# Kernel tuning notes

Measured on AMD Instinct MI355X. Metric: run time of the kernel, lower is better.

## Reference

```python
import jax, jax.numpy as jnp
import numpy as np

BEV_H, BEV_W = 200, 200
X_RANGE = (-50.0, 50.0)
Y_RANGE = (-50.0, 50.0)
IMG_W, IMG_H = 1600.0, 928.0
EPS = 1e-6


def _bev_points():
    x_half = (X_RANGE[1] - X_RANGE[0]) / (2 * BEV_W)
    y_half = (Y_RANGE[1] - Y_RANGE[0]) / (2 * BEV_H)
    xs = jnp.linspace(X_RANGE[0] + x_half, X_RANGE[1] - x_half, BEV_W)
    ys = jnp.linspace(Y_RANGE[0] + y_half, Y_RANGE[1] - y_half, BEV_H)
    gy, gx = jnp.meshgrid(ys, xs, indexing='ij')
    return jnp.stack([gx, gy, jnp.zeros_like(gx)], -1).reshape(-1, 3)  # (P,3)


def _bilinear_zeros(fm, x, y):
    # fm: (C,H,W); x,y: (P,) pixel coords; grid_sample bilinear, zeros padding, align_corners=True
    H, W = fm.shape[1], fm.shape[2]
    x0 = jnp.floor(x); y0 = jnp.floor(y)
    wx = x - x0; wy = y - y0
    def g(xi, yi):
        ok = ((xi >= 0) & (xi <= W - 1) & (yi >= 0) & (yi <= H - 1)).astype(fm.dtype)
        xc = jnp.clip(xi, 0, W - 1).astype(jnp.int32)
        yc = jnp.clip(yi, 0, H - 1).astype(jnp.int32)
        return fm[:, yc, xc] * ok  # (C,P)
    v00 = g(x0, y0); v01 = g(x0 + 1, y0); v10 = g(x0, y0 + 1); v11 = g(x0 + 1, y0 + 1)
    return v00 * (1 - wx) * (1 - wy) + v01 * wx * (1 - wy) + v10 * (1 - wx) * wy + v11 * wx * wy


def _bev_forward(feats, intrinsics, extrinsics, conv_w, conv_b, bn_gamma, bn_beta, bn_mean, bn_var):
    B, N, C, fH, fW = feats.shape
    pts = _bev_points()                                   # (P,3), z=0 ground plane
    E = jnp.linalg.inv(extrinsics)                        # T_ego->cam (B,N,4,4)
    R = E[..., :3, :3]; t = E[..., :3, 3]
    pts_cam = jnp.einsum('bnij,pj->bnpi', R, pts) + t[:, :, None, :]  # (B,N,P,3)
    depth = pts_cam[..., 2]
    p_img = jnp.einsum('bnij,bnpj->bnpi', intrinsics, pts_cam)
    u = p_img[..., 0] / (p_img[..., 2] + EPS)
    v = p_img[..., 1] / (p_img[..., 2] + EPS)
    u_feat = u * (fW / IMG_W); v_feat = v * (fH / IMG_H)
    u_norm = u_feat / (fW - 1.0) * 2.0 - 1.0
    v_norm = v_feat / (fH - 1.0) * 2.0 - 1.0
    valid = ((depth > 0.1) & (u_norm >= -1.0) & (u_norm <= 1.0)
             & (v_norm >= -1.0) & (v_norm <= 1.0)).astype(feats.dtype)  # (B,N,P)
    # align_corners=True: pixel coords recover u_feat/v_feat
    xs = (u_norm + 1.0) * 0.5 * (fW - 1.0)
    ys = (v_norm + 1.0) * 0.5 * (fH - 1.0)
    P = BEV_H * BEV_W
    bev_sum = jnp.zeros((B, C, P), feats.dtype)
    valid_sum = jnp.zeros((B, 1, P), feats.dtype)
    sample_b = jax.vmap(_bilinear_zeros)
    for cam in range(N):  # small fixed camera loop, as in original
        s = sample_b(feats[:, cam], xs[:, cam], ys[:, cam])  # (B,C,P)
        vb = valid[:, cam][:, None, :]
        bev_sum = bev_sum + s * vb
        valid_sum = valid_sum + vb
    bev = (bev_sum / (valid_sum + EPS)).reshape(B, C, BEV_H, BEV_W)
    # 1x1 conv + inference BatchNorm + ReLU
    y = jnp.einsum('oc,bchw->bohw', conv_w, bev) + conv_b[:, None, None]
    y = (y - bn_mean[:, None, None]) / jnp.sqrt(bn_var[:, None, None] + 1e-5)
    y = y * bn_gamma[:, None, None] + bn_beta[:, None, None]
    return jax.nn.relu(y)


def setup_inputs() -> dict:
    key = jax.random.key(0)
    ks = jax.random.split(key, 6)
    B, N, C, fH, fW = 4, 6, 256, 29, 50
    feats = jax.random.normal(ks[0], (B, N, C, fH, fW), jnp.float32)
    # intrinsics: realistic pinhole K
    fx = 1266.0 + 20.0 * jax.random.normal(ks[1], (B, N), jnp.float32)
    fy = 1266.0 + 20.0 * jax.random.normal(ks[2], (B, N), jnp.float32)
    z = jnp.zeros((B, N), jnp.float32); o = jnp.ones((B, N), jnp.float32)
    K = jnp.stack([jnp.stack([fx, z, 800.0 * o], -1),
                   jnp.stack([z, fy, 464.0 * o], -1),
                   jnp.stack([z, z, o], -1)], -2)  # (B,N,3,3)
    # extrinsics: proper SE(3) T_cam->ego (random rotation via QR + translation)
    A = jax.random.normal(ks[3], (B, N, 3, 3), jnp.float32)
    Q, _ = jnp.linalg.qr(A)
    Q = jnp.where(jnp.linalg.det(Q)[..., None, None] < 0, -Q, Q)
    tr = jax.random.uniform(ks[4], (B, N, 3), jnp.float32, -2.0, 2.0)
    E = jnp.zeros((B, N, 4, 4), jnp.float32)
    E = E.at[..., :3, :3].set(Q).at[..., :3, 3].set(tr).at[..., 3, 3].set(1.0)
    conv_w = 0.05 * jax.random.normal(ks[5], (C, C), jnp.float32)
    return {
        'feats': feats, 'intrinsics': K, 'extrinsics': E,
        'conv_w': conv_w, 'conv_b': jnp.zeros((C,), jnp.float32),
        'bn_gamma': jnp.ones((C,), jnp.float32), 'bn_beta': jnp.zeros((C,), jnp.float32),
        'bn_mean': jnp.zeros((C,), jnp.float32), 'bn_var': jnp.ones((C,), jnp.float32),
    }


def reference(feats, intrinsics, extrinsics, conv_w, conv_b, bn_gamma, bn_beta, bn_mean, bn_var):
    return _bev_forward(feats, intrinsics, extrinsics, conv_w, conv_b,
                        bn_gamma, bn_beta, bn_mean, bn_var)
```

## Files before the change

### kernel.cpp

```cpp
#include <hip/hip_runtime.h>
#include <hip/hip_bf16.h>


#define P_TOT  40000
#define FH     29
#define FW     50
#define NCAM   6

typedef short bf16x8 __attribute__((ext_vector_type(8)));
typedef float f32x4  __attribute__((ext_vector_type(4)));
typedef unsigned short u16x8 __attribute__((ext_vector_type(8)));

__device__ __forceinline__ float bf2f(unsigned short u) {
    union { unsigned int i; float f; } x; x.i = ((unsigned int)u) << 16; return x.f;
}
__device__ __forceinline__ unsigned short f2bf(float f) {
    union { float f; unsigned int i; } x; x.f = f;
    unsigned int i = x.i;
    return (unsigned short)((i + 0x7FFFu + ((i >> 16) & 1u)) >> 16);
}

__global__ void prep_kernel(const float* __restrict__ K, const float* __restrict__ E,
                            const float* __restrict__ convw, const float* __restrict__ convb,
                            const float* __restrict__ gamma, const float* __restrict__ beta,
                            const float* __restrict__ mean, const float* __restrict__ var,
                            float* __restrict__ params, float* __restrict__ sb,
                            unsigned short* __restrict__ wbf) {
    int idx = blockIdx.x * 256 + threadIdx.x;
    wbf[idx] = f2bf(convw[idx]);
    if (blockIdx.x != 0) return;
    int o = threadIdx.x;
    float rstd = rsqrtf(var[o] + 1e-5f);
    float s = gamma[o] * rstd;
    sb[o]       = s;
    sb[256 + o] = (convb[o] - mean[o]) * s + beta[o];
    if (o >= 24) return;
    const float* e = E + o * 16;
    const float* k = K + o * 9;
    float a00=e[0], a01=e[1], a02=e[2],  t0=e[3];
    float a10=e[4], a11=e[5], a12=e[6],  t1=e[7];
    float a20=e[8], a21=e[9], a22=e[10], t2=e[11];
    float c00 =  (a11*a22 - a12*a21);
    float c01 = -(a10*a22 - a12*a20);
    float c02 =  (a10*a21 - a11*a20);
    float det = a00*c00 + a01*c01 + a02*c02;
    float id = 1.0f / det;
    float i00 =  c00*id;
    float i01 = -(a01*a22 - a02*a21)*id;
    float i02 =  (a01*a12 - a02*a11)*id;
    float i10 =  c01*id;
    float i11 =  (a00*a22 - a02*a20)*id;
    float i12 = -(a00*a12 - a02*a10)*id;
    float i20 =  c02*id;
    float i21 = -(a00*a21 - a01*a20)*id;
    float i22 =  (a00*a11 - a01*a10)*id;
    float tp0 = -(i00*t0 + i01*t1 + i02*t2);
    float tp1 = -(i10*t0 + i11*t1 + i12*t2);
    float tp2 = -(i20*t0 + i21*t1 + i22*t2);
    float* q = params + o * 12;
    q[0] = k[0]*i00 + k[1]*i10 + k[2]*i20;
    q[1] = k[0]*i01 + k[1]*i11 + k[2]*i21;
    q[2] = k[0]*tp0 + k[1]*tp1 + k[2]*tp2;
    q[3] = k[3]*i00 + k[4]*i10 + k[5]*i20;
    q[4] = k[3]*i01 + k[4]*i11 + k[5]*i21;
    q[5] = k[3]*tp0 + k[4]*tp1 + k[5]*tp2;
    q[6] = k[6]*i00 + k[7]*i10 + k[8]*i20;
    q[7] = k[6]*i01 + k[7]*i11 + k[8]*i21;
    q[8] = k[6]*tp0 + k[7]*tp1 + k[8]*tp2;
    q[9]  = i20;
    q[10] = i21;
    q[11] = tp2;
}

__global__ __launch_bounds__(256) void transpose_kernel(const float* __restrict__ feats,
                                                        unsigned short* __restrict__ ft) {
    __shared__ unsigned short tile[256][58];
    int by = blockIdx.x;
    int t  = threadIdx.x;
    int bn = by / FH, y = by - bn * FH;
    const float* src = feats + (size_t)bn * 256 * FH * FW + y * FW;
    #pragma unroll
    for (int i = 0; i < 50; ++i) {
        int flat = i * 256 + t;
        int c = flat / 50;
        int x = flat - c * 50;
        tile[c][x] = f2bf(src[c * FH * FW + x]);
    }
    __syncthreads();
    unsigned short* dst = ft + (size_t)by * 50 * 256;
    #pragma unroll
    for (int i = 0; i < 25; ++i) {
        int flat = i * 512 + t * 2;
        int x = flat >> 8;
        int c = flat & 255;
        unsigned int v = (unsigned int)tile[c][x] | ((unsigned int)tile[c + 1][x] << 16);
        *(unsigned int*)(dst + x * 256 + c) = v;
    }
}

__global__ __launch_bounds__(512, 4) void fused_kernel(const unsigned short* __restrict__ ft,
                                                       const float* __restrict__ params,
                                                       const unsigned short* __restrict__ wbf,
                                                       const float* __restrict__ sb,
                                                       float* __restrict__ out) {
    __shared__ unsigned short Bt[64][264];
    __shared__ unsigned short Wt[2][256][40];
    __shared__ int           sbf[64][6];
    __shared__ unsigned int  swxy[64][6];
    __shared__ int           scnt[64];
    __shared__ float         sscale[64];
    __shared__ float         ssb[512];

    int tid   = threadIdx.x;
    int pbase = blockIdx.x * 64;
    int b     = blockIdx.y;

    ssb[tid] = sb[tid];

    {
        int row = tid >> 1, half = tid & 1;
        const unsigned short* s = wbf + row * 256 + half * 16;
        uint4 w0 = *(const uint4*)(s);
        uint4 w1 = *(const uint4*)(s + 8);
        *(uint4*)&Wt[0][row][half * 16]     = w0;
        *(uint4*)&Wt[0][row][half * 16 + 8] = w1;
    }

    if (tid < 384) {
        int pt  = tid / 6;
        int cam = tid - pt * 6;
        int p   = pbase + pt;
        float gx = -49.75f + 0.5f * (float)(p % 200);
        float gy = -49.75f + 0.5f * (float)(p / 200);
        const float* q = params + (b * NCAM + cam) * 12;
        float wh    = q[6] * gx + q[7]  * gy + q[8];
        float depth = q[9] * gx + q[10] * gy + q[11];
        float inv = 1.0f / (wh + 1e-6f);
        float u = (q[0] * gx + q[1] * gy + q[2]) * inv;
        float v = (q[3] * gx + q[4] * gy + q[5]) * inv;
        float un = u * (50.0f / 1600.0f) * (2.0f / 49.0f) - 1.0f;
        float vn = v * (29.0f / 928.0f)  * (2.0f / 28.0f) - 1.0f;
        int bf = -1; unsigned int wxy = 0;
        if (depth > 0.1f && un >= -1.0f && un <= 1.0f &&
                            vn >= -1.0f && vn <= 1.0f) {
            float xs = (un + 1.0f) * 0.5f * 49.0f;
            float ys = (vn + 1.0f) * 0.5f * 28.0f;
            float x0f = floorf(xs), y0f = floorf(ys);
            float wx = xs - x0f, wy = ys - y0f;
            int x0 = (int)x0f, y0 = (int)y0f;
            int okx = (x0 < FW - 1) ? 1 : 0;
            int oky = (y0 < FH - 1) ? 2 : 0;
            int base = (((b * NCAM + cam) * FH + y0) * FW + x0) * 256;
            bf  = base | okx | oky;
            wxy = (unsigned int)(wx * 65535.0f + 0.5f)
                | ((unsigned int)(wy * 65535.0f + 0.5f) << 16);
        }
        sbf[pt][cam]  = bf;
        swxy[pt][cam] = wxy;
    }
    __syncthreads();

    if (tid < 64) {
        int c = 0;
        #pragma unroll
        for (int cam = 0; cam < NCAM; ++cam) {
            int v = sbf[tid][cam];
            unsigned int w = swxy[tid][cam];
            if (v >= 0) { sbf[tid][c] = v; swxy[tid][c] = w; ++c; }
        }
        scnt[tid]   = c;
        sscale[tid] = 1.0f / ((float)c + 1e-6f);
    }
    __syncthreads();

    {
        int pt = tid >> 3, sub = tid & 7, ch0 = sub * 32;
        float acc[32];
        #pragma unroll
        for (int j = 0; j < 32; ++j) acc[j] = 0.0f;
        int n = scnt[pt];
        for (int s = 0; s < n; ++s) {
            int bf = sbf[pt][s];
            unsigned int wxy = swxy[pt][s];
            int base = bf & ~255;
            int okx = bf & 1, oky = bf & 2;
            float wx = (float)(wxy & 0xffffu) * (1.0f / 65535.0f);
            float wy = (float)(wxy >> 16)     * (1.0f / 65535.0f);
            float iwx = 1.0f - wx, iwy = 1.0f - wy;
            float w00 = iwx * iwy;
            float w01 = okx ? wx * iwy : 0.0f;
            float w10 = oky ? iwx * wy : 0.0f;
            float w11 = (okx && oky) ? wx * wy : 0.0f;
            const unsigned short* p00 = ft + base + ch0;
            int o01 = okx ? 256 : 0;
            int o10 = oky ? FW * 256 : 0;
            #pragma unroll
            for (int qv = 0; qv < 4; ++qv) {
                u16x8 v0 = *(const u16x8*)(p00 + qv * 8);
                #pragma unroll
                for (int j = 0; j < 8; ++j) acc[qv * 8 + j] += w00 * bf2f(v0[j]);
            }
            #pragma unroll
            for (int qv = 0; qv < 4; ++qv) {
                u16x8 v1 = *(const u16x8*)(p00 + o01 + qv * 8);
                #pragma unroll
                for (int j = 0; j < 8; ++j) acc[qv * 8 + j] += w01 * bf2f(v1[j]);
            }
            #pragma unroll
            for (int qv = 0; qv < 4; ++qv) {
                u16x8 v2 = *(const u16x8*)(p00 + o10 + qv * 8);
                #pragma unroll
                for (int j = 0; j < 8; ++j) acc[qv * 8 + j] += w10 * bf2f(v2[j]);
            }
            #pragma unroll
            for (int qv = 0; qv < 4; ++qv) {
                u16x8 v3 = *(const u16x8*)(p00 + o10 + o01 + qv * 8);
                #pragma unroll
                for (int j = 0; j < 8; ++j) acc[qv * 8 + j] += w11 * bf2f(v3[j]);
            }
        }
        float sc = sscale[pt];
        #pragma unroll
        for (int qv = 0; qv < 4; ++qv) {
            u16x8 ov;
            #pragma unroll
            for (int j = 0; j < 8; ++j) ov[j] = f2bf(acc[qv * 8 + j] * sc);
            *(u16x8*)&Bt[pt][ch0 + qv * 8] = ov;
        }
    }
    __syncthreads();

    int lane = tid & 63, wv = tid >> 6;
    f32x4 acc2[2][4];
    #pragma unroll
    for (int f = 0; f < 2; ++f)
        #pragma unroll
        for (int nf = 0; nf < 4; ++nf) acc2[f][nf] = (f32x4){0.f, 0.f, 0.f, 0.f};
    int arow = wv * 32 + (lane & 15);
    int kq   = (lane >> 4) * 8;
    int srow = tid >> 1, shalf = tid & 1;
    for (int kt = 0; kt < 8; ++kt) {
        uint4 w0, w1;
        if (kt < 7) {
            const unsigned short* s = wbf + srow * 256 + (kt + 1) * 32 + shalf * 16;
            w0 = *(const uint4*)(s);
            w1 = *(const uint4*)(s + 8);
        }
        bf16x8 a0 = *(const bf16x8*)&Wt[kt & 1][arow][kq];
        bf16x8 a1 = *(const bf16x8*)&Wt[kt & 1][arow + 16][kq];
        #pragma unroll
        for (int nf = 0; nf < 4; ++nf) {
            bf16x8 bb = *(const bf16x8*)&Bt[nf * 16 + (lane & 15)][kt * 32 + kq];
            acc2[0][nf] = __builtin_amdgcn_mfma_f32_16x16x32_bf16(a0, bb, acc2[0][nf], 0, 0, 0);
            acc2[1][nf] = __builtin_amdgcn_mfma_f32_16x16x32_bf16(a1, bb, acc2[1][nf], 0, 0, 0);
        }
        if (kt < 7) {
            *(uint4*)&Wt[(kt + 1) & 1][srow][shalf * 16]     = w0;
            *(uint4*)&Wt[(kt + 1) & 1][srow][shalf * 16 + 8] = w1;
        }
        __syncthreads();
    }
    #pragma unroll
    for (int f = 0; f < 2; ++f) {
        #pragma unroll
        for (int nf = 0; nf < 4; ++nf) {
            #pragma unroll
            for (int r = 0; r < 4; ++r) {
                int o = wv * 32 + f * 16 + (lane >> 4) * 4 + r;
                float y = acc2[f][nf][r] * ssb[o] + ssb[256 + o];
                out[((size_t)(b * 256 + o)) * P_TOT + pbase + nf * 16 + (lane & 15)]
                    = fmaxf(y, 0.0f);
            }
        }
    }
}

extern "C" void kernel_launch(void* const* d_in, const int* in_sizes, int n_in,
                              void* d_out, int out_size, void* d_ws, size_t ws_size,
                              hipStream_t stream) {
    const float* feats = (const float*)d_in[0];
    const float* intr  = (const float*)d_in[1];
    const float* extr  = (const float*)d_in[2];
    const float* convw = (const float*)d_in[3];
    const float* convb = (const float*)d_in[4];
    const float* gamma = (const float*)d_in[5];
    const float* beta  = (const float*)d_in[6];
    const float* mean  = (const float*)d_in[7];
    const float* var   = (const float*)d_in[8];

    char* ws = (char*)d_ws;
    float*          params = (float*)(ws + 0);
    float*          sb     = (float*)(ws + 2048);
    unsigned short* wbf    = (unsigned short*)(ws + 4096);
    unsigned short* ft     = (unsigned short*)(ws + 135168);
    float* out = (float*)d_out;

    hipLaunchKernelGGL(prep_kernel, dim3(256), dim3(256), 0, stream,
                       intr, extr, convw, convb, gamma, beta, mean, var, params, sb, wbf);
    hipLaunchKernelGGL(transpose_kernel, dim3(696), dim3(256), 0, stream, feats, ft);
    hipLaunchKernelGGL(fused_kernel, dim3(625, 4), dim3(512), 0, stream,
                       ft, params, wbf, sb, out);
}
```

Measured before the change: 77.15 us.

## Merge prep into transpose kernel and read conv weights directly from global

After: 88.37 us. +14.5%, slower.

```diff
diff --git a/kernel.cpp b/kernel.cpp
--- a/kernel.cpp
+++ b/kernel.cpp
@@ -20,64 +20,66 @@
     return (unsigned short)((i + 0x7FFFu + ((i >> 16) & 1u)) >> 16);
 }
 
-__global__ void prep_kernel(const float* __restrict__ K, const float* __restrict__ E,
-                            const float* __restrict__ convw, const float* __restrict__ convb,
-                            const float* __restrict__ gamma, const float* __restrict__ beta,
-                            const float* __restrict__ mean, const float* __restrict__ var,
-                            float* __restrict__ params, float* __restrict__ sb,
-                            unsigned short* __restrict__ wbf) {
-    int idx = blockIdx.x * 256 + threadIdx.x;
-    wbf[idx] = f2bf(convw[idx]);
-    if (blockIdx.x != 0) return;
-    int o = threadIdx.x;
-    float rstd = rsqrtf(var[o] + 1e-5f);
-    float s = gamma[o] * rstd;
-    sb[o]       = s;
-    sb[256 + o] = (convb[o] - mean[o]) * s + beta[o];
-    if (o >= 24) return;
-    const float* e = E + o * 16;
-    const float* k = K + o * 9;
-    float a00=e[0], a01=e[1], a02=e[2],  t0=e[3];
-    float a10=e[4], a11=e[5], a12=e[6],  t1=e[7];
-    float a20=e[8], a21=e[9], a22=e[10], t2=e[11];
-    float c00 =  (a11*a22 - a12*a21);
-    float c01 = -(a10*a22 - a12*a20);
-    float c02 =  (a10*a21 - a11*a20);
-    float det = a00*c00 + a01*c01 + a02*c02;
-    float id = 1.0f / det;
-    float i00 =  c00*id;
-    float i01 = -(a01*a22 - a02*a21)*id;
-    float i02 =  (a01*a12 - a02*a11)*id;
-    float i10 =  c01*id;
-    float i11 =  (a00*a22 - a02*a20)*id;
-    float i12 = -(a00*a12 - a02*a10)*id;
-    float i20 =  c02*id;
-    float i21 = -(a00*a21 - a01*a20)*id;
-    float i22 =  (a00*a11 - a01*a10)*id;
-    float tp0 = -(i00*t0 + i01*t1 + i02*t2);
-    float tp1 = -(i10*t0 + i11*t1 + i12*t2);
-    float tp2 = -(i20*t0 + i21*t1 + i22*t2);
-    float* q = params + o * 12;
-    q[0] = k[0]*i00 + k[1]*i10 + k[2]*i20;
-    q[1] = k[0]*i01 + k[1]*i11 + k[2]*i21;
-    q[2] = k[0]*tp0 + k[1]*tp1 + k[2]*tp2;
-    q[3] = k[3]*i00 + k[4]*i10 + k[5]*i20;
-    q[4] = k[3]*i01 + k[4]*i11 + k[5]*i21;
-    q[5] = k[3]*tp0 + k[4]*tp1 + k[5]*tp2;
-    q[6] = k[6]*i00 + k[7]*i10 + k[8]*i20;
-    q[7] = k[6]*i01 + k[7]*i11 + k[8]*i21;
-    q[8] = k[6]*tp0 + k[7]*tp1 + k[8]*tp2;
-    q[9]  = i20;
-    q[10] = i21;
-    q[11] = tp2;
-}
-
-__global__ __launch_bounds__(256) void transpose_kernel(const float* __restrict__ feats,
-                                                        unsigned short* __restrict__ ft) {
+__global__ __launch_bounds__(256) void prep_transpose_kernel(
+        const float* __restrict__ feats, const float* __restrict__ K,
+        const float* __restrict__ E, const float* __restrict__ convw,
+        const float* __restrict__ convb, const float* __restrict__ gamma,
+        const float* __restrict__ beta, const float* __restrict__ mean,
+        const float* __restrict__ var, float* __restrict__ params,
+        float* __restrict__ sb, unsigned short* __restrict__ wbf,
+        unsigned short* __restrict__ ft) {
     __shared__ unsigned short tile[256][58];
-    int by = blockIdx.x;
-    int t  = threadIdx.x;
-    int bn = by / FH, y = by - bn * FH;
+    int blk = blockIdx.x;
+    int t   = threadIdx.x;
+    if (blk < 256) {
+        int idx = blk * 256 + t;
+        wbf[idx] = f2bf(convw[idx]);
+    }
+    if (blk == 696) {
+        int o = t;
+        float rstd = rsqrtf(var[o] + 1e-5f);
+        float s = gamma[o] * rstd;
+        sb[o]       = s;
+        sb[256 + o] = (convb[o] - mean[o]) * s + beta[o];
+        if (o >= 24) return;
+        const float* e = E + o * 16;
+        const float* k = K + o * 9;
+        float a00=e[0], a01=e[1], a02=e[2],  t0=e[3];
+        float a10=e[4], a11=e[5], a12=e[6],  t1=e[7];
+        float a20=e[8], a21=e[9], a22=e[10], t2=e[11];
+        float c00 =  (a11*a22 - a12*a21);
+        float c01 = -(a10*a22 - a12*a20);
+        float c02 =  (a10*a21 - a11*a20);
+        float det = a00*c00 + a01*c01 + a02*c02;
+        float id = 1.0f / det;
+        float i00 =  c00*id;
+        float i01 = -(a01*a22 - a02*a21)*id;
+        float i02 =  (a01*a12 - a02*a11)*id;
+        float i10 =  c01*id;
+        float i11 =  (a00*a22 - a02*a20)*id;
+        float i12 = -(a00*a12 - a02*a10)*id;
+        float i20 =  c02*id;
+        float i21 = -(a00*a21 - a01*a20)*id;
+        float i22 =  (a00*a11 - a01*a10)*id;
+        float tp0 = -(i00*t0 + i01*t1 + i02*t2);
+        float tp1 = -(i10*t0 + i11*t1 + i12*t2);
+        float tp2 = -(i20*t0 + i21*t1 + i22*t2);
+        float* q = params + o * 12;
+        q[0] = k[0]*i00 + k[1]*i10 + k[2]*i20;
+        q[1] = k[0]*i01 + k[1]*i11 + k[2]*i21;
+        q[2] = k[0]*tp0 + k[1]*tp1 + k[2]*tp2;
+        q[3] = k[3]*i00 + k[4]*i10 + k[5]*i20;
+        q[4] = k[3]*i01 + k[4]*i11 + k[5]*i21;
+        q[5] = k[3]*tp0 + k[4]*tp1 + k[5]*tp2;
+        q[6] = k[6]*i00 + k[7]*i10 + k[8]*i20;
+        q[7] = k[6]*i01 + k[7]*i11 + k[8]*i21;
+        q[8] = k[6]*tp0 + k[7]*tp1 + k[8]*tp2;
+        q[9]  = i20;
+        q[10] = i21;
+        q[11] = tp2;
+        return;
+    }
+    int bn = blk / FH, y = blk - bn * FH;
     const float* src = feats + (size_t)bn * 256 * FH * FW + y * FW;
     #pragma unroll
     for (int i = 0; i < 50; ++i) {
@@ -87,7 +89,7 @@
         tile[c][x] = f2bf(src[c * FH * FW + x]);
     }
     __syncthreads();
-    unsigned short* dst = ft + (size_t)by * 50 * 256;
+    unsigned short* dst = ft + (size_t)blk * 50 * 256;
     #pragma unroll
     for (int i = 0; i < 25; ++i) {
         int flat = i * 512 + t * 2;
@@ -98,13 +100,12 @@
     }
 }
 
-__global__ __launch_bounds__(512, 4) void fused_kernel(const unsigned short* __restrict__ ft,
+__global__ __launch_bounds__(512, 6) void fused_kernel(const unsigned short* __restrict__ ft,
                                                        const float* __restrict__ params,
                                                        const unsigned short* __restrict__ wbf,
                                                        const float* __restrict__ sb,
                                                        float* __restrict__ out) {
     __shared__ unsigned short Bt[64][264];
-    __shared__ unsigned short Wt[2][256][40];
     __shared__ int           sbf[64][6];
     __shared__ unsigned int  swxy[64][6];
     __shared__ int           scnt[64];
@@ -116,15 +117,6 @@
     int b     = blockIdx.y;
 
     ssb[tid] = sb[tid];
-
-    {
-        int row = tid >> 1, half = tid & 1;
-        const unsigned short* s = wbf + row * 256 + half * 16;
-        uint4 w0 = *(const uint4*)(s);
-        uint4 w1 = *(const uint4*)(s + 8);
-        *(uint4*)&Wt[0][row][half * 16]     = w0;
-        *(uint4*)&Wt[0][row][half * 16 + 8] = w1;
-    }
 
     if (tid < 384) {
         int pt  = tid / 6;
@@ -238,27 +230,17 @@
         for (int nf = 0; nf < 4; ++nf) acc2[f][nf] = (f32x4){0.f, 0.f, 0.f, 0.f};
     int arow = wv * 32 + (lane & 15);
     int kq   = (lane >> 4) * 8;
-    int srow = tid >> 1, shalf = tid & 1;
+    const unsigned short* wptr = wbf + arow * 256 + kq;
+    #pragma unroll
     for (int kt = 0; kt < 8; ++kt) {
-        uint4 w0, w1;
-        if (kt < 7) {
-            const unsigned short* s = wbf + srow * 256 + (kt + 1) * 32 + shalf * 16;
-            w0 = *(const uint4*)(s);
-            w1 = *(const uint4*)(s + 8);
-        }
-        bf16x8 a0 = *(const bf16x8*)&Wt[kt & 1][arow][kq];
-        bf16x8 a1 = *(const bf16x8*)&Wt[kt & 1][arow + 16][kq];
+        bf16x8 a0 = *(const bf16x8*)(wptr + kt * 32);
+        bf16x8 a1 = *(const bf16x8*)(wptr + 16 * 256 + kt * 32);
         #pragma unroll
         for (int nf = 0; nf < 4; ++nf) {
             bf16x8 bb = *(const bf16x8*)&Bt[nf * 16 + (lane & 15)][kt * 32 + kq];
             acc2[0][nf] = __builtin_amdgcn_mfma_f32_16x16x32_bf16(a0, bb, acc2[0][nf], 0, 0, 0);
             acc2[1][nf] = __builtin_amdgcn_mfma_f32_16x16x32_bf16(a1, bb, acc2[1][nf], 0, 0, 0);
         }
-        if (kt < 7) {
-            *(uint4*)&Wt[(kt + 1) & 1][srow][shalf * 16]     = w0;
-            *(uint4*)&Wt[(kt + 1) & 1][srow][shalf * 16 + 8] = w1;
-        }
-        __syncthreads();
     }
     #pragma unroll
     for (int f = 0; f < 2; ++f) {
@@ -295,9 +277,9 @@
     unsigned short* ft     = (unsigned short*)(ws + 135168);
     float* out = (float*)d_out;
 
-    hipLaunchKernelGGL(prep_kernel, dim3(256), dim3(256), 0, stream,
-                       intr, extr, convw, convb, gamma, beta, mean, var, params, sb, wbf);
-    hipLaunchKernelGGL(transpose_kernel, dim3(696), dim3(256), 0, stream, feats, ft);
+    hipLaunchKernelGGL(prep_transpose_kernel, dim3(697), dim3(256), 0, stream,
+                       feats, intr, extr, convw, convb, gamma, beta, mean, var,
+                       params, sb, wbf, ft);
     hipLaunchKernelGGL(fused_kernel, dim3(625, 4), dim3(512), 0, stream,
                        ft, params, wbf, sb, out);
 }
```
